# Kernel optimization log

Hardware: AMD Instinct MI355X
Metric: run time of the kernel (lower is better)

Reference implementation:

```python
import jax, jax.numpy as jnp
import numpy as np

BEV_H, BEV_W, ED, HEADS, HD, LEVELS, POINTS, LAYERS = 200, 200, 128, 8, 16, 4, 8, 2
SPATIAL = [(128, 256), (64, 128), (32, 64), (16, 32)]
NV = sum(h * w for h, w in SPATIAL)
NQ = BEV_H * BEV_W
NCLS = 21


def setup_inputs() -> dict:
    key = jax.random.key(0)
    ks = iter(jax.random.split(key, 48))
    r = lambda shape, s=0.02: jax.random.normal(next(ks), shape, jnp.float32) * s
    inp = dict(
        value=r((1, NV, ED), 1.0),
        bev_queries=r((NQ, ED), 0.02),
        bev_pos=r((NQ, ED), 0.02),
        proj_indices=jax.random.randint(next(ks), (1, BEV_H, BEV_W), 0, 250000),
        Wv=r((LAYERS, ED, ED)), bv=jnp.zeros((LAYERS, ED)),
        Woff=r((LAYERS, ED, HEADS * LEVELS * POINTS * 2), 0.01),
        boff=jnp.zeros((LAYERS, HEADS * LEVELS * POINTS * 2)),
        Wattn=r((LAYERS, ED, HEADS * LEVELS * POINTS), 0.01),
        battn=jnp.zeros((LAYERS, HEADS * LEVELS * POINTS)),
        Wout=r((LAYERS, ED, ED)), bout=jnp.zeros((LAYERS, ED)),
        Wf1=r((LAYERS, ED, ED)), bf1=jnp.zeros((LAYERS, ED)),
        Wf2=r((LAYERS, ED, ED)), bf2=jnp.zeros((LAYERS, ED)),
        ln_g=jnp.ones((LAYERS, 2, ED)), ln_b=jnp.zeros((LAYERS, 2, ED)),
        cw1=r((128, ED, 7, 7), 0.01), g1=jnp.ones(128), b1=jnp.zeros(128),
        cw2=r((64, 128, 3, 3), 0.02), g2=jnp.ones(64), b2=jnp.zeros(64),
        cw3=r((48, 64, 3, 3), 0.02), g3=jnp.ones(48), b3=jnp.zeros(48),
        cw4=r((48, 48, 3, 3), 0.02), g4=jnp.ones(48), b4=jnp.zeros(48),
        objw=r((NCLS, 48, 1, 1), 0.05), objb=jnp.zeros(NCLS),
    )
    return inp


def _ln(x, g, b):
    m = x.mean(-1, keepdims=True)
    v = ((x - m) ** 2).mean(-1, keepdims=True)
    return (x - m) * jax.lax.rsqrt(v + 1e-5) * g + b


def _deform_attn(q, value, Wv, bv, Woff, boff, Wattn, battn, Wout, bout, ref):
    # multi-scale deformable attention (Deformable-DETR / BEVFormer core)
    v = (value[0] @ Wv + bv).reshape(NV, HEADS, HD)
    off = (q @ Woff + boff).reshape(NQ, HEADS, LEVELS, POINTS, 2)
    attn = jax.nn.softmax((q @ Wattn + battn).reshape(NQ, HEADS, LEVELS * POINTS), -1)
    attn = attn.reshape(NQ, HEADS, LEVELS, POINTS)
    out = jnp.zeros((HEADS, NQ, HD), jnp.float32)
    start = 0
    for l, (H, W) in enumerate(SPATIAL):
        vl = v[start:start + H * W].transpose(1, 0, 2)  # [HEADS, H*W, HD]
        start += H * W
        # normalized sampling locations in [0,1]
        loc = ref[:, None, None, :] + off[:, :, l] / jnp.array([W, H], jnp.float32)
        x = loc[..., 0] * W - 0.5  # grid_sample align_corners=False convention
        y = loc[..., 1] * H - 0.5  # [NQ, HEADS, POINTS]
        x0 = jnp.floor(x)
        y0 = jnp.floor(y)
        acc = jnp.zeros((HEADS, NQ, POINTS, HD), jnp.float32)
        for dx, dy in ((0, 0), (1, 0), (0, 1), (1, 1)):
            xc = x0 + dx
            yc = y0 + dy
            wgt = (1.0 - jnp.abs(x - xc)) * (1.0 - jnp.abs(y - yc))
            valid = (xc >= 0) & (xc < W) & (yc >= 0) & (yc < H)
            xi = jnp.clip(xc, 0, W - 1).astype(jnp.int32)
            yi = jnp.clip(yc, 0, H - 1).astype(jnp.int32)
            idx = (yi * W + xi).transpose(1, 0, 2)  # [HEADS, NQ, POINTS]
            g = jax.vmap(lambda vh, ih: vh[ih])(vl, idx)  # [HEADS, NQ, POINTS, HD]
            acc = acc + (wgt * valid).transpose(1, 0, 2)[..., None] * g
        out = out + jnp.einsum('nhp,hnpd->hnd', attn[:, :, l], acc)
    return out.transpose(1, 0, 2).reshape(NQ, ED) @ Wout + bout


def _bev_encoder(bev_queries, bev_pos, value, Wv, bv, Woff, boff, Wattn, battn, Wout, bout, Wf1, bf1, Wf2, bf2, ln_g, ln_b):
    gx = (jnp.arange(BEV_W, dtype=jnp.float32) + 0.5) / BEV_W
    gy = (jnp.arange(BEV_H, dtype=jnp.float32) + 0.5) / BEV_H
    ref = jnp.stack(jnp.meshgrid(gx, gy), -1).reshape(NQ, 2)  # (x, y)
    q = bev_queries
    for i in range(LAYERS):  # operation_order: cross_attn, norm, ffn, norm
        a = _deform_attn(q + bev_pos, value, Wv[i], bv[i], Woff[i], boff[i],
                         Wattn[i], battn[i], Wout[i], bout[i], ref)
        q = _ln(q + a, ln_g[i, 0], ln_b[i, 0])
        h = jax.nn.relu(q @ Wf1[i] + bf1[i]) @ Wf2[i] + bf2[i]
        q = _ln(q + h, ln_g[i, 1], ln_b[i, 1])
    return q


def _conv(x, w, p):
    return jax.lax.conv_general_dilated(x, w, (1, 1), [(p, p), (p, p)],
                                        dimension_numbers=('NCHW', 'OIHW', 'NCHW'))


def _bn_relu(x, g, b):
    m = x.mean((0, 2, 3), keepdims=True)
    v = x.var((0, 2, 3), keepdims=True)
    return jax.nn.relu((x - m) * jax.lax.rsqrt(v + 1e-5) * g[None, :, None, None] + b[None, :, None, None])


def reference(value, bev_queries, bev_pos, proj_indices, Wv, bv, Woff, boff, Wattn, battn, Wout, bout, Wf1, bf1, Wf2, bf2, ln_g, ln_b, cw1, g1, b1, cw2, g2, b2, cw3, g3, b3, cw4, g4, b4, objw, objb):
    observed_masks = proj_indices < jnp.max(proj_indices)  # mask_update
    q = _bev_encoder(bev_queries, bev_pos, value, Wv, bv, Woff, boff, Wattn, battn,
                     Wout, bout, Wf1, bf1, Wf2, bf2, ln_g, ln_b)
    mem = q.reshape(1, BEV_H, BEV_W, ED).transpose(0, 3, 1, 2)  # [1, ED, H, W]
    h = _bn_relu(_conv(mem, cw1, 3), g1, b1)
    h = _bn_relu(_conv(h, cw2, 1), g2, b2)
    h = _bn_relu(_conv(h, cw3, 1), g3, b3)
    h = _bn_relu(_conv(h, cw4, 1), g4, b4)
    semmap = _conv(h, objw, 0) + objb[None, :, None, None]
    return semmap, observed_masks
```

## Files before the change

kernel.cpp:

```cpp
#include <hip/hip_runtime.h>
#include <cstdint>
#include <cstddef>

#define NQ 40000
#define EDIM 128
#define NVAL 43520
#define NCLS 21

typedef unsigned short u16;
typedef unsigned int uint;
typedef short bf16x8 __attribute__((ext_vector_type(8)));
typedef float f32x4 __attribute__((ext_vector_type(4)));

__device__ inline u16 f2b(float f) {
    unsigned u = __float_as_uint(f);
    unsigned r = u + 0x7FFF + ((u >> 16) & 1);
    return (u16)(r >> 16);
}
__device__ inline float b2f(u16 v) {
    unsigned u = ((unsigned)v) << 16;
    return __uint_as_float(u);
}
__device__ inline float blo(uint u) { return __uint_as_float(u << 16); }
__device__ inline float bhi(uint u) { return __uint_as_float(u & 0xFFFF0000u); }

__global__ void reduce_max_int(const int* __restrict__ idx, int* __restrict__ mx) {
    int i = blockIdx.x * 256 + threadIdx.x;
    int v = (i < NQ) ? idx[i] : 0;
    for (int o = 32; o > 0; o >>= 1) v = max(v, __shfl_xor(v, o, 64));
    if ((threadIdx.x & 63) == 0) atomicMax(mx, v);
}

__global__ void write_mask(const int* __restrict__ idx, const int* __restrict__ mx,
                           float* __restrict__ out) {
    int i = blockIdx.x * 256 + threadIdx.x;
    if (i >= NQ) return;
    out[i] = (idx[i] < *mx) ? 1.0f : 0.0f;
}

__global__ void cvt_b_k(const float* __restrict__ src, u16* __restrict__ dst, int n8) {
    int i = blockIdx.x * 256 + threadIdx.x;
    if (i >= n8) return;
    const float4 a = ((const float4*)src)[i * 2];
    const float4 b = ((const float4*)src)[i * 2 + 1];
    u16 o[8] = {f2b(a.x), f2b(a.y), f2b(a.z), f2b(a.w), f2b(b.x), f2b(b.y), f2b(b.z), f2b(b.w)};
    ((uint4*)dst)[i] = *(const uint4*)o;
}

__global__ void add2b_k(const float* __restrict__ a, const float* __restrict__ b,
                        u16* __restrict__ c, int n8) {
    int i = blockIdx.x * 256 + threadIdx.x;
    if (i >= n8) return;
    const float4 a0 = ((const float4*)a)[i * 2], a1 = ((const float4*)a)[i * 2 + 1];
    const float4 b0 = ((const float4*)b)[i * 2], b1 = ((const float4*)b)[i * 2 + 1];
    u16 o[8] = {f2b(a0.x + b0.x), f2b(a0.y + b0.y), f2b(a0.z + b0.z), f2b(a0.w + b0.w),
                f2b(a1.x + b1.x), f2b(a1.y + b1.y), f2b(a1.z + b1.z), f2b(a1.w + b1.w)};
    ((uint4*)c)[i] = *(const uint4*)o;
}

__global__ void pack_enc_k(const float* __restrict__ Wv, const float* __restrict__ Woff,
                           const float* __restrict__ Wattn, const float* __restrict__ Wout,
                           const float* __restrict__ Wf1, const float* __restrict__ Wf2,
                           u16* __restrict__ dst) {
    int i = blockIdx.x * 256 + threadIdx.x;
    if (i >= 327680) return;
    int l = i / 163840, r = i % 163840;
    int k = r / 1280, col = r % 1280;
    const float* src; int N; int n; u16* d;
    u16* base = dst + (size_t)l * 163840;
    if (col < 128)       { src = Wv    + (size_t)l * 16384; N = 128; n = col;        d = base;          }
    else if (col < 640)  { src = Woff  + (size_t)l * 65536; N = 512; n = col - 128;  d = base + 16384;  }
    else if (col < 896)  { src = Wattn + (size_t)l * 32768; N = 256; n = col - 640;  d = base + 81920;  }
    else if (col < 1024) { src = Wout  + (size_t)l * 16384; N = 128; n = col - 896;  d = base + 114688; }
    else if (col < 1152) { src = Wf1   + (size_t)l * 16384; N = 128; n = col - 1024; d = base + 131072; }
    else                 { src = Wf2   + (size_t)l * 16384; N = 128; n = col - 1152; d = base + 147456; }
    d[(size_t)n * 128 + k] = f2b(src[(size_t)k * N + n]);
}

__global__ void pack_bias_k(const float* __restrict__ boff, const float* __restrict__ battn,
                            float* __restrict__ dst) {
    int i = blockIdx.x * 256 + threadIdx.x;
    if (i >= 1536) return;
    int l = i / 768, r = i % 768;
    dst[i] = (r < 512) ? boff[(size_t)l * 512 + r] : battn[(size_t)l * 256 + r - 512];
}

__global__ void pack_cw_k(const float* __restrict__ w, u16* __restrict__ wT,
                          int OC, int IC, int KS, int OCp, int ICp) {
    int i = blockIdx.x * 256 + threadIdx.x;
    int tot = KS * KS * OCp * ICp;
    if (i >= tot) return;
    int ic = i % ICp; int r = i / ICp;
    int oc = r % OCp; int tap = r / OCp;
    int ky = tap / KS, kx = tap % KS;
    float v = 0.f;
    if (oc < OC && ic < IC)
        v = w[(((size_t)oc * IC + ic) * KS + ky) * KS + kx];
    wT[i] = f2b(v);
}

__global__ __launch_bounds__(256) void gemm_mfma_k(
        const u16* __restrict__ A, const u16* __restrict__ BT,
        const float* __restrict__ bias, float* __restrict__ Cf,
        u16* __restrict__ Cb, int N, int relu) {
    __shared__ u16 As[64 * 136];
    __shared__ u16 Bs[64 * 136];
    const int m0 = blockIdx.x * 64, n0 = blockIdx.y * 64;
    const int t = threadIdx.x;
#pragma unroll
    for (int ci = t; ci < 1024; ci += 256) {
        int r = ci >> 4, c = ci & 15;
        *(uint4*)&As[r * 136 + c * 8] = *(const uint4*)&A[(size_t)(m0 + r) * 128 + c * 8];
        *(uint4*)&Bs[r * 136 + c * 8] = *(const uint4*)&BT[(size_t)(n0 + r) * 128 + c * 8];
    }
    __syncthreads();
    const int wave = t >> 6, lane = t & 63;
    const int wm = (wave & 1) * 32, wn = (wave >> 1) * 32;
    const int lr = lane & 15, lk = (lane >> 4) * 8;
    f32x4 acc[2][2] = {};
#pragma unroll
    for (int ks = 0; ks < 4; ks++) {
        bf16x8 a0 = *(const bf16x8*)&As[(wm + lr) * 136 + ks * 32 + lk];
        bf16x8 a1 = *(const bf16x8*)&As[(wm + 16 + lr) * 136 + ks * 32 + lk];
        bf16x8 b0 = *(const bf16x8*)&Bs[(wn + lr) * 136 + ks * 32 + lk];
        bf16x8 b1 = *(const bf16x8*)&Bs[(wn + 16 + lr) * 136 + ks * 32 + lk];
        acc[0][0] = __builtin_amdgcn_mfma_f32_16x16x32_bf16(a0, b0, acc[0][0], 0, 0, 0);
        acc[0][1] = __builtin_amdgcn_mfma_f32_16x16x32_bf16(a0, b1, acc[0][1], 0, 0, 0);
        acc[1][0] = __builtin_amdgcn_mfma_f32_16x16x32_bf16(a1, b0, acc[1][0], 0, 0, 0);
        acc[1][1] = __builtin_amdgcn_mfma_f32_16x16x32_bf16(a1, b1, acc[1][1], 0, 0, 0);
    }
    float bj0 = bias[n0 + wn + lr];
    float bj1 = bias[n0 + wn + 16 + lr];
#pragma unroll
    for (int i = 0; i < 2; i++) {
#pragma unroll
        for (int j = 0; j < 2; j++) {
            float bb = j ? bj1 : bj0;
#pragma unroll
            for (int r = 0; r < 4; r++) {
                int ml = wm + i * 16 + (lane >> 4) * 4 + r;
                int nl = wn + j * 16 + lr;
                float v = acc[i][j][r] + bb;
                if (relu) v = fmaxf(v, 0.f);
                size_t o = (size_t)(m0 + ml) * N + n0 + nl;
                if (Cf) Cf[o] = v;
                if (Cb) Cb[o] = f2b(v);
            }
        }
    }
}

template <int KS, int ICP>
__global__ __launch_bounds__(256) void conv4_mfma_k(
        const u16* __restrict__ pimg, const u16* __restrict__ wT,
        float* __restrict__ out, int OCtot) {
    constexpr int PAD = KS / 2;
    constexpr int WIN = 64 + KS - 1;
    constexpr int LDSTR = ICP + 8;
    constexpr int KSTEPS = ICP / 32;
    constexpr int NTAP = KS * KS;
    __shared__ u16 As[WIN * LDSTR];
    const int bx = blockIdx.x;
    const int y = bx >> 2;
    const int xc = bx & 3;
    const int x0 = (xc == 3) ? 136 : xc * 64;
    const int n0 = blockIdx.y * 64;
    const int t = threadIdx.x;
    const int wave = t >> 6, lane = t & 63;
    const int wm = (wave & 1) * 32, wn = (wave >> 1) * 32;
    const int lr = lane & 15, lkq = lane >> 4, lk = lkq * 8;

    f32x4 acc[2][2] = {};
    const u16* wbase = wT + (size_t)n0 * ICP;

    bf16x8 cur0[KSTEPS], cur1[KSTEPS], nxt0[KSTEPS], nxt1[KSTEPS];
#pragma unroll
    for (int ks = 0; ks < KSTEPS; ks++) {
        cur0[ks] = *(const bf16x8*)&wbase[(size_t)(wn + lr) * ICP + ks * 32 + lk];
        cur1[ks] = *(const bf16x8*)&wbase[(size_t)(wn + 16 + lr) * ICP + ks * 32 + lk];
    }

    for (int ky = 0; ky < KS; ky++) {
        __syncthreads();
        const u16* src = pimg + (((size_t)(y + ky + 3 - PAD)) * 208 + (x0 + 3 - PAD)) * ICP;
        for (int ci = t; ci < WIN * (ICP / 8); ci += 256) {
            int r = ci / (ICP / 8), c = ci - r * (ICP / 8);
            *(uint4*)&As[r * LDSTR + c * 8] = *(const uint4*)&src[(size_t)r * ICP + c * 8];
        }
        __syncthreads();
#pragma unroll
        for (int kx = 0; kx < KS; kx++) {
            const int tap = ky * KS + kx;
            if (tap + 1 < NTAP) {
                const u16* wb = wbase + (size_t)(tap + 1) * OCtot * ICP;
#pragma unroll
                for (int ks = 0; ks < KSTEPS; ks++) {
                    nxt0[ks] = *(const bf16x8*)&wb[(size_t)(wn + lr) * ICP + ks * 32 + lk];
                    nxt1[ks] = *(const bf16x8*)&wb[(size_t)(wn + 16 + lr) * ICP + ks * 32 + lk];
                }
            }
#pragma unroll
            for (int ks = 0; ks < KSTEPS; ks++) {
                bf16x8 a0 = *(const bf16x8*)&As[(wm + lr + kx) * LDSTR + ks * 32 + lk];
                bf16x8 a1 = *(const bf16x8*)&As[(wm + 16 + lr + kx) * LDSTR + ks * 32 + lk];
                acc[0][0] = __builtin_amdgcn_mfma_f32_16x16x32_bf16(a0, cur0[ks], acc[0][0], 0, 0, 0);
                acc[0][1] = __builtin_amdgcn_mfma_f32_16x16x32_bf16(a0, cur1[ks], acc[0][1], 0, 0, 0);
                acc[1][0] = __builtin_amdgcn_mfma_f32_16x16x32_bf16(a1, cur0[ks], acc[1][0], 0, 0, 0);
                acc[1][1] = __builtin_amdgcn_mfma_f32_16x16x32_bf16(a1, cur1[ks], acc[1][1], 0, 0, 0);
            }
#pragma unroll
            for (int ks = 0; ks < KSTEPS; ks++) { cur0[ks] = nxt0[ks]; cur1[ks] = nxt1[ks]; }
        }
    }
    const int px0 = y * 200 + x0;
#pragma unroll
    for (int i = 0; i < 2; i++) {
#pragma unroll
        for (int j = 0; j < 2; j++) {
#pragma unroll
            for (int r = 0; r < 4; r++) {
                int ml = wm + i * 16 + lkq * 4 + r;
                int nl = wn + j * 16 + lr;
                out[(size_t)(px0 + ml) * OCtot + n0 + nl] = acc[i][j][r];
            }
        }
    }
}

__global__ __launch_bounds__(256) void deform3_k(
        const u16* __restrict__ v, const u16* __restrict__ oa,
        u16* __restrict__ outb, int q0, int nq) {
    const int t = threadIdx.x;
    const int wq = t >> 6;
    const int lane = t & 63;
    const int s = lane >> 5;
    const int l32 = lane & 31;
    const int h = l32 >> 2;
    const int cl = l32 & 3;
    const int qi = blockIdx.x * 8 + wq * 2 + s;
    if (qi >= nq) return;
    const int gq = q0 + qi;
    const float rx = ((gq % 200) + 0.5f) / 200.f;
    const float ry = ((gq / 200) + 0.5f) / 200.f;

    const uint* lp = (const uint*)(oa + (size_t)qi * 768 + 512 + h * 32);
    float lg[32];
#pragma unroll
    for (int i = 0; i < 16; i++) { uint u = lp[i]; lg[2 * i] = blo(u); lg[2 * i + 1] = bhi(u); }
    float mx = -1e30f;
#pragma unroll
    for (int i = 0; i < 32; i++) mx = fmaxf(mx, lg[i]);
    float ssum = 0.f;
#pragma unroll
    for (int i = 0; i < 32; i++) { lg[i] = __expf(lg[i] - mx); ssum += lg[i]; }
    const float inv = 1.f / ssum;

    const uint* op = (const uint*)(oa + (size_t)qi * 768 + h * 64);

    const int HS[4] = {128, 64, 32, 16};
    const int WS[4] = {256, 128, 64, 32};
    const int ST[4] = {0, 32768, 40960, 43008};
    float a0 = 0.f, a1 = 0.f, a2 = 0.f, a3 = 0.f;
#pragma unroll
    for (int l = 0; l < 4; l++) {
        const int H = HS[l], W = WS[l];
        const float fW = (float)W, fH = (float)H;
        const u16* vb = v + (size_t)ST[l] * 128 + h * 16 + cl * 4;
#pragma unroll
        for (int p = 0; p < 8; p++) {
            uint pr = op[l * 8 + p];
            float ox = blo(pr), oy = bhi(pr);
            float xx = rx * fW + ox - 0.5f;
            float yy = ry * fH + oy - 0.5f;
            float xf = floorf(xx), yf = floorf(yy);
            int ix = (int)xf, iy = (int)yf;
            float fx = xx - xf, fy = yy - yf;
            float aw = lg[l * 8 + p] * inv;
            int x1 = ix + 1, y1 = iy + 1;
            bool vx0 = (unsigned)ix < (unsigned)W;
            bool vx1 = (unsigned)x1 < (unsigned)W;
            bool vy0 = (unsigned)iy < (unsigned)H;
            bool vy1 = (unsigned)y1 < (unsigned)H;
            int cx0 = min(max(ix, 0), W - 1), cx1 = min(max(x1, 0), W - 1);
            int cy0 = min(max(iy, 0), H - 1), cy1 = min(max(y1, 0), H - 1);
            float w00 = (vx0 && vy0) ? (1.f - fx) * (1.f - fy) * aw : 0.f;
            float w10 = (vx1 && vy0) ? fx * (1.f - fy) * aw : 0.f;
            float w01 = (vx0 && vy1) ? (1.f - fx) * fy * aw : 0.f;
            float w11 = (vx1 && vy1) ? fx * fy * aw : 0.f;
            uint2 u00 = *(const uint2*)(vb + (size_t)(cy0 * W + cx0) * 128);
            uint2 u10 = *(const uint2*)(vb + (size_t)(cy0 * W + cx1) * 128);
            uint2 u01 = *(const uint2*)(vb + (size_t)(cy1 * W + cx0) * 128);
            uint2 u11 = *(const uint2*)(vb + (size_t)(cy1 * W + cx1) * 128);
            a0 = fmaf(w00, blo(u00.x), a0); a1 = fmaf(w00, bhi(u00.x), a1);
            a2 = fmaf(w00, blo(u00.y), a2); a3 = fmaf(w00, bhi(u00.y), a3);
            a0 = fmaf(w10, blo(u10.x), a0); a1 = fmaf(w10, bhi(u10.x), a1);
            a2 = fmaf(w10, blo(u10.y), a2); a3 = fmaf(w10, bhi(u10.y), a3);
            a0 = fmaf(w01, blo(u01.x), a0); a1 = fmaf(w01, bhi(u01.x), a1);
            a2 = fmaf(w01, blo(u01.y), a2); a3 = fmaf(w01, bhi(u01.y), a3);
            a0 = fmaf(w11, blo(u11.x), a0); a1 = fmaf(w11, bhi(u11.x), a1);
            a2 = fmaf(w11, blo(u11.y), a2); a3 = fmaf(w11, bhi(u11.y), a3);
        }
    }
    uint2 o;
    o.x = (uint)f2b(a0) | ((uint)f2b(a1) << 16);
    o.y = (uint)f2b(a2) | ((uint)f2b(a3) << 16);
    *(uint2*)(outb + (size_t)gq * 128 + h * 16 + cl * 4) = o;
}

__global__ __launch_bounds__(256) void add_ln_k(
        float* __restrict__ q, const float* __restrict__ a,
        const float* __restrict__ g, const float* __restrict__ b,
        u16* __restrict__ qb) {
    const int row = blockIdx.x * 4 + (threadIdx.x >> 6);
    const int lane = threadIdx.x & 63;
    float s0 = q[(size_t)row * 128 + lane] + a[(size_t)row * 128 + lane];
    float s1 = q[(size_t)row * 128 + 64 + lane] + a[(size_t)row * 128 + 64 + lane];
    float sum = s0 + s1;
    for (int o = 32; o > 0; o >>= 1) sum += __shfl_xor(sum, o, 64);
    float mean = sum * (1.f / 128.f);
    float d0 = s0 - mean, d1 = s1 - mean;
    float vs = d0 * d0 + d1 * d1;
    for (int o = 32; o > 0; o >>= 1) vs += __shfl_xor(vs, o, 64);
    float inv = rsqrtf(vs * (1.f / 128.f) + 1e-5f);
    float o0 = d0 * inv * g[lane] + b[lane];
    float o1 = d1 * inv * g[64 + lane] + b[64 + lane];
    q[(size_t)row * 128 + lane] = o0;
    q[(size_t)row * 128 + 64 + lane] = o1;
    qb[(size_t)row * 128 + lane] = f2b(o0);
    qb[(size_t)row * 128 + 64 + lane] = f2b(o1);
}

__global__ void fill_pimg2_k(const u16* __restrict__ qb, u16* __restrict__ pimg) {
    int i = blockIdx.x * 256 + threadIdx.x;
    if (i >= 685568) return;
    int pp = i >> 4, c8 = i & 15;
    int py = pp / 208, px = pp - py * 208;
    uint4 val = {0u, 0u, 0u, 0u};
    if (py >= 3 && py < 203 && px >= 3 && px < 203)
        val = ((const uint4*)qb)[((size_t)((py - 3) * 200 + (px - 3))) * 16 + c8];
    ((uint4*)pimg)[i] = val;
}

__global__ __launch_bounds__(256) void bn_stats2_k(const float* __restrict__ x,
                                                   float* __restrict__ acc,
                                                   int cSh, int ppb) {
    const int t = threadIdx.x;
    const int Cp = 1 << cSh;
    const int c = t & (Cp - 1);
    const int sub = t >> cSh;
    const int nsub = 256 >> cSh;
    float s = 0.f, s2 = 0.f;
    const int pbase = blockIdx.x * ppb;
    for (int i = sub; i < ppb; i += nsub) {
        float v = x[(size_t)(pbase + i) * Cp + c];
        s += v; s2 += v * v;
    }
    __shared__ float ls[256], ls2[256];
    ls[t] = s; ls2[t] = s2;
    __syncthreads();
    if (t < Cp) {
        for (int k = 1; k < nsub; k++) { s += ls[t + k * Cp]; s2 += ls2[t + k * Cp]; }
        atomicAdd(&acc[2 * t], s);
        atomicAdd(&acc[2 * t + 1], s2);
    }
}

__global__ void bn_fin_k(const float* __restrict__ acc, float* __restrict__ mv, int C) {
    int t = threadIdx.x;
    if (t >= C) return;
    float m = acc[2 * t] * (1.f / 40000.f);
    float var = acc[2 * t + 1] * (1.f / 40000.f) - m * m;
    mv[2 * t] = m;
    mv[2 * t + 1] = rsqrtf(var + 1e-5f);
}

__global__ void bn_apply_pad2_k(const float* __restrict__ x, const float* __restrict__ mv,
                                const float* __restrict__ g, const float* __restrict__ b,
                                u16* __restrict__ outp, int cSh, int Creal) {
    int i = blockIdx.x * 256 + threadIdx.x;
    int Cp = 1 << cSh;
    if (i >= 206 * 208 * Cp) return;
    int c = i & (Cp - 1);
    int pp = i >> cSh;
    int py = pp / 208, px = pp - py * 208;
    float v = 0.f;
    if (c < Creal && py >= 3 && py < 203 && px >= 3 && px < 203) {
        int p = (py - 3) * 200 + (px - 3);
        v = fmaxf((x[(size_t)p * Cp + c] - mv[2 * c]) * mv[2 * c + 1] * g[c] + b[c], 0.f);
    }
    outp[i] = f2b(v);
}

__global__ void bn_apply2_k(const float* __restrict__ x, const float* __restrict__ mv,
                            const float* __restrict__ g, const float* __restrict__ b,
                            u16* __restrict__ outb, int cSh, int Creal) {
    int i = blockIdx.x * 256 + threadIdx.x;
    int Cp = 1 << cSh;
    if (i >= 40000 * Cp) return;
    int c = i & (Cp - 1);
    float v = 0.f;
    if (c < Creal) v = fmaxf((x[i] - mv[2 * c]) * mv[2 * c + 1] * g[c] + b[c], 0.f);
    outb[i] = f2b(v);
}

__global__ void obj_conv_k(const u16* __restrict__ in, const float* __restrict__ w,
                           const float* __restrict__ bias, float* __restrict__ out) {
    int p = blockIdx.x * 256 + threadIdx.x;
    if (p >= 40000) return;
    float xin[48];
#pragma unroll
    for (int c = 0; c < 48; c++) xin[c] = b2f(in[(size_t)p * 64 + c]);
    for (int o = 0; o < NCLS; o++) {
        float acc = bias[o];
#pragma unroll
        for (int c = 0; c < 48; c++) acc += xin[c] * w[o * 48 + c];
        out[(size_t)o * 40000 + p] = acc;
    }
}

extern "C" void kernel_launch(void* const* d_in, const int* in_sizes, int n_in,
                              void* d_out, int out_size, void* d_ws, size_t ws_size,
                              hipStream_t stream) {
    const float* value   = (const float*)d_in[0];
    const float* bev_q   = (const float*)d_in[1];
    const float* bev_pos = (const float*)d_in[2];
    const int*   proj    = (const int*)d_in[3];
    const float* Wv      = (const float*)d_in[4];
    const float* bv      = (const float*)d_in[5];
    const float* Woff    = (const float*)d_in[6];
    const float* boff    = (const float*)d_in[7];
    const float* Wattn   = (const float*)d_in[8];
    const float* battn   = (const float*)d_in[9];
    const float* Wout    = (const float*)d_in[10];
    const float* bout    = (const float*)d_in[11];
    const float* Wf1     = (const float*)d_in[12];
    const float* bf1     = (const float*)d_in[13];
    const float* Wf2     = (const float*)d_in[14];
    const float* bf2     = (const float*)d_in[15];
    const float* ln_g    = (const float*)d_in[16];
    const float* ln_b    = (const float*)d_in[17];
    const float* cw1     = (const float*)d_in[18];
    const float* g1      = (const float*)d_in[19];
    const float* b1      = (const float*)d_in[20];
    const float* cw2     = (const float*)d_in[21];
    const float* g2      = (const float*)d_in[22];
    const float* b2      = (const float*)d_in[23];
    const float* cw3     = (const float*)d_in[24];
    const float* g3      = (const float*)d_in[25];
    const float* b3      = (const float*)d_in[26];
    const float* cw4     = (const float*)d_in[27];
    const float* g4      = (const float*)d_in[28];
    const float* b4      = (const float*)d_in[29];
    const float* objw    = (const float*)d_in[30];
    const float* objb    = (const float*)d_in[31];
    float* out = (float*)d_out;

    float* WSb = (float*)d_ws;
    float* q     = WSb + 0;
    u16*   qb    = (u16*)(WSb + 5120000);
    u16*   qpb   = (u16*)(WSb + 7680000);
    u16*   valb  = (u16*)(WSb + 10240000);
    u16*   vbufb = (u16*)(WSb + 13025280);
    u16*   fb    = (u16*)(WSb + 15810560);
    float* tmp   = WSb + 18882560;
    u16*   aob   = (u16*)(WSb + 24002560);
    u16*   hb    = (u16*)(WSb + 26562560);
    u16*   wenc  = (u16*)(WSb + 29122560);
    u16*   wcv   = (u16*)(WSb + 29286400);
    float* bnacc = WSb + 29761536;
    float* bnmv  = WSb + 29762048;
    int*   maxi  = (int*)(WSb + 29762304);
    float* fbias = WSb + 29762308;

    u16*   pimg = (u16*)(WSb + 10240000);
    float* c1f  = tmp;
    u16*   c1b  = (u16*)(WSb + 13025280);
    float* c2f  = WSb + 0;
    u16*   c2b  = (u16*)(WSb + 5120000);
    float* c3f  = WSb + 2560000;
    u16*   c3b  = (u16*)(WSb + 7680000);
    float* c4f  = WSb + 0;
    u16*   c4b  = (u16*)(WSb + 15810560);

    const size_t L = 163840;
    u16* WvT[2]; u16* WoffT[2]; u16* WoutT[2]; u16* Wf1T[2]; u16* Wf2T[2];
    for (int l = 0; l < 2; l++) {
        u16* base = wenc + l * L;
        WvT[l]    = base;
        WoffT[l]  = base + 16384;
        WoutT[l]  = base + 114688;
        Wf1T[l]   = base + 131072;
        Wf2T[l]   = base + 147456;
    }
    u16* w1T = wcv;
    u16* w2T = wcv + 802816;
    u16* w3T = wcv + 876544;
    u16* w4T = wcv + 913408;

    hipMemsetAsync(maxi, 0, sizeof(int), stream);
    reduce_max_int<<<157, 256, 0, stream>>>(proj, maxi);
    write_mask<<<157, 256, 0, stream>>>(proj, maxi, out + 840000);

    pack_enc_k<<<1280, 256, 0, stream>>>(Wv, Woff, Wattn, Wout, Wf1, Wf2, wenc);
    pack_bias_k<<<6, 256, 0, stream>>>(boff, battn, fbias);
    pack_cw_k<<<3136, 256, 0, stream>>>(cw1, w1T, 128, 128, 7, 128, 128);
    pack_cw_k<<<288, 256, 0, stream>>>(cw2, w2T, 64, 128, 3, 64, 128);
    pack_cw_k<<<144, 256, 0, stream>>>(cw3, w3T, 48, 64, 3, 64, 64);
    pack_cw_k<<<144, 256, 0, stream>>>(cw4, w4T, 48, 48, 3, 64, 64);
    cvt_b_k<<<2720, 256, 0, stream>>>(value, valb, NVAL * 128 / 8);

    hipMemcpyAsync(q, bev_q, (size_t)NQ * EDIM * sizeof(float),
                   hipMemcpyDeviceToDevice, stream);
    const int CH0 = 19968, CH1 = 20032;
    for (int l = 0; l < 2; l++) {
        gemm_mfma_k<<<dim3(680, 2), 256, 0, stream>>>(
            valb, WvT[l], bv + (size_t)l * 128, nullptr, vbufb, 128, 0);
        add2b_k<<<2500, 256, 0, stream>>>(q, bev_pos, qpb, NQ * 128 / 8);
        for (int cidx = 0; cidx < 2; cidx++) {
            int qs = cidx ? CH0 : 0;
            int nq = cidx ? CH1 : CH0;
            gemm_mfma_k<<<dim3(nq / 64, 12), 256, 0, stream>>>(
                qpb + (size_t)qs * 128, WoffT[l], fbias + (size_t)l * 768,
                nullptr, fb, 768, 0);
            deform3_k<<<nq / 8, 256, 0, stream>>>(vbufb, fb, aob, qs, nq);
        }
        gemm_mfma_k<<<dim3(625, 2), 256, 0, stream>>>(
            aob, WoutT[l], bout + (size_t)l * 128, tmp, nullptr, 128, 0);
        add_ln_k<<<10000, 256, 0, stream>>>(q, tmp, ln_g + (size_t)(l * 2 + 0) * 128,
                                            ln_b + (size_t)(l * 2 + 0) * 128, qb);
        gemm_mfma_k<<<dim3(625, 2), 256, 0, stream>>>(
            qb, Wf1T[l], bf1 + (size_t)l * 128, nullptr, hb, 128, 1);
        gemm_mfma_k<<<dim3(625, 2), 256, 0, stream>>>(
            hb, Wf2T[l], bf2 + (size_t)l * 128, tmp, nullptr, 128, 0);
        add_ln_k<<<10000, 256, 0, stream>>>(q, tmp, ln_g + (size_t)(l * 2 + 1) * 128,
                                            ln_b + (size_t)(l * 2 + 1) * 128, qb);
    }

    fill_pimg2_k<<<2678, 256, 0, stream>>>(qb, pimg);

    conv4_mfma_k<7, 128><<<dim3(800, 2), 256, 0, stream>>>(pimg, w1T, c1f, 128);
    hipMemsetAsync(bnacc, 0, 512 * sizeof(float), stream);
    bn_stats2_k<<<125, 256, 0, stream>>>(c1f, bnacc, 7, 320);
    bn_fin_k<<<1, 128, 0, stream>>>(bnacc, bnmv, 128);
    bn_apply_pad2_k<<<21424, 256, 0, stream>>>(c1f, bnmv, g1, b1, c1b, 7, 128);

    conv4_mfma_k<3, 128><<<dim3(800, 1), 256, 0, stream>>>(c1b, w2T, c2f, 64);
    hipMemsetAsync(bnacc, 0, 512 * sizeof(float), stream);
    bn_stats2_k<<<125, 256, 0, stream>>>(c2f, bnacc, 6, 320);
    bn_fin_k<<<1, 64, 0, stream>>>(bnacc, bnmv, 64);
    bn_apply_pad2_k<<<10712, 256, 0, stream>>>(c2f, bnmv, g2, b2, c2b, 6, 64);

    conv4_mfma_k<3, 64><<<dim3(800, 1), 256, 0, stream>>>(c2b, w3T, c3f, 64);
    hipMemsetAsync(bnacc, 0, 512 * sizeof(float), stream);
    bn_stats2_k<<<125, 256, 0, stream>>>(c3f, bnacc, 6, 320);
    bn_fin_k<<<1, 48, 0, stream>>>(bnacc, bnmv, 48);
    bn_apply_pad2_k<<<10712, 256, 0, stream>>>(c3f, bnmv, g3, b3, c3b, 6, 48);

    conv4_mfma_k<3, 64><<<dim3(800, 1), 256, 0, stream>>>(c3b, w4T, c4f, 64);
    hipMemsetAsync(bnacc, 0, 512 * sizeof(float), stream);
    bn_stats2_k<<<125, 256, 0, stream>>>(c4f, bnacc, 6, 320);
    bn_fin_k<<<1, 48, 0, stream>>>(bnacc, bnmv, 48);
    bn_apply2_k<<<10000, 256, 0, stream>>>(c4f, bnmv, g4, b4, c4b, 6, 48);

    obj_conv_k<<<157, 256, 0, stream>>>(c4b, objw, objb, out);
}
```

Before: 1.161 ms.

## Process two output rows per conv block and stage weights in double-buffered LDS

The implicit-GEMM conv kernel now computes two output rows per block (grid halved). Each wave owns one row and 64 pixels by 32 output channels. Per-tap weight tiles are now loaded cooperatively into a double-buffered LDS buffer instead of each wave loading its own fragments into registers, so each weight tile is fetched once per block and reused across both rows. The cost is more LDS use, an extra barrier per tap, fewer blocks for occupancy and more accumulator registers per thread.

```diff
diff --git a/kernel.cpp b/kernel.cpp
--- a/kernel.cpp
+++ b/kernel.cpp
@@ -151,75 +151,98 @@
 }
 
 template <int KS, int ICP>
-__global__ __launch_bounds__(256) void conv4_mfma_k(
+__global__ __launch_bounds__(256) void conv5_mfma_k(
         const u16* __restrict__ pimg, const u16* __restrict__ wT,
         float* __restrict__ out, int OCtot) {
     constexpr int PAD = KS / 2;
     constexpr int WIN = 64 + KS - 1;
-    constexpr int LDSTR = ICP + 8;
+    constexpr int STR = ICP + 8;
     constexpr int KSTEPS = ICP / 32;
     constexpr int NTAP = KS * KS;
-    __shared__ u16 As[WIN * LDSTR];
+    constexpr int ACH = WIN * (ICP / 8);
+    constexpr int NB = ICP / 32;
+    __shared__ u16 As[2 * WIN * STR];
+    __shared__ u16 Bs[2 * 64 * STR];
     const int bx = blockIdx.x;
-    const int y = bx >> 2;
+    const int yp = (bx >> 2) * 2;
     const int xc = bx & 3;
     const int x0 = (xc == 3) ? 136 : xc * 64;
     const int n0 = blockIdx.y * 64;
     const int t = threadIdx.x;
     const int wave = t >> 6, lane = t & 63;
-    const int wm = (wave & 1) * 32, wn = (wave >> 1) * 32;
+    const int row = wave >> 1;
+    const int wn = (wave & 1) * 32;
     const int lr = lane & 15, lkq = lane >> 4, lk = lkq * 8;
 
-    f32x4 acc[2][2] = {};
+    f32x4 acc[4][2] = {};
     const u16* wbase = wT + (size_t)n0 * ICP;
 
-    bf16x8 cur0[KSTEPS], cur1[KSTEPS], nxt0[KSTEPS], nxt1[KSTEPS];
-#pragma unroll
-    for (int ks = 0; ks < KSTEPS; ks++) {
-        cur0[ks] = *(const bf16x8*)&wbase[(size_t)(wn + lr) * ICP + ks * 32 + lk];
-        cur1[ks] = *(const bf16x8*)&wbase[(size_t)(wn + 16 + lr) * ICP + ks * 32 + lk];
-    }
+    uint4 breg[NB];
+    int bro[NB], bco[NB];
+#pragma unroll
+    for (int k = 0; k < NB; k++) {
+        int ci = t + k * 256;
+        bro[k] = ci / (ICP / 8);
+        bco[k] = ci - bro[k] * (ICP / 8);
+    }
+#pragma unroll
+    for (int k = 0; k < NB; k++)
+        breg[k] = *(const uint4*)&wbase[(size_t)bro[k] * ICP + bco[k] * 8];
+#pragma unroll
+    for (int k = 0; k < NB; k++)
+        *(uint4*)&Bs[(size_t)bro[k] * STR + bco[k] * 8] = breg[k];
 
     for (int ky = 0; ky < KS; ky++) {
         __syncthreads();
-        const u16* src = pimg + (((size_t)(y + ky + 3 - PAD)) * 208 + (x0 + 3 - PAD)) * ICP;
-        for (int ci = t; ci < WIN * (ICP / 8); ci += 256) {
-            int r = ci / (ICP / 8), c = ci - r * (ICP / 8);
-            *(uint4*)&As[r * LDSTR + c * 8] = *(const uint4*)&src[(size_t)r * ICP + c * 8];
+        {
+            const u16* s0 = pimg + (((size_t)(yp + ky + 3 - PAD)) * 208 + (x0 + 3 - PAD)) * ICP;
+            const u16* s1 = pimg + (((size_t)(yp + 1 + ky + 3 - PAD)) * 208 + (x0 + 3 - PAD)) * ICP;
+            for (int ci = t; ci < 2 * ACH; ci += 256) {
+                int w2 = ci / ACH, rem = ci - w2 * ACH;
+                int r = rem / (ICP / 8), c = rem - r * (ICP / 8);
+                const u16* s = w2 ? s1 : s0;
+                *(uint4*)&As[(size_t)(w2 * WIN + r) * STR + c * 8] =
+                    *(const uint4*)&s[(size_t)r * ICP + c * 8];
+            }
         }
-        __syncthreads();
-#pragma unroll
         for (int kx = 0; kx < KS; kx++) {
             const int tap = ky * KS + kx;
+            __syncthreads();
             if (tap + 1 < NTAP) {
-                const u16* wb = wbase + (size_t)(tap + 1) * OCtot * ICP;
-#pragma unroll
-                for (int ks = 0; ks < KSTEPS; ks++) {
-                    nxt0[ks] = *(const bf16x8*)&wb[(size_t)(wn + lr) * ICP + ks * 32 + lk];
-                    nxt1[ks] = *(const bf16x8*)&wb[(size_t)(wn + 16 + lr) * ICP + ks * 32 + lk];
+                const u16* ws = wbase + (size_t)(tap + 1) * OCtot * ICP;
+#pragma unroll
+                for (int k = 0; k < NB; k++)
+                    breg[k] = *(const uint4*)&ws[(size_t)bro[k] * ICP + bco[k] * 8];
+            }
+            const u16* ab = &As[((size_t)row * WIN + kx) * STR];
+            const u16* bb = &Bs[(size_t)((tap & 1) * 64 + wn) * STR];
+#pragma unroll
+            for (int ks = 0; ks < KSTEPS; ks++) {
+                bf16x8 b0 = *(const bf16x8*)&bb[(size_t)lr * STR + ks * 32 + lk];
+                bf16x8 b1 = *(const bf16x8*)&bb[(size_t)(lr + 16) * STR + ks * 32 + lk];
+#pragma unroll
+                for (int i = 0; i < 4; i++) {
+                    bf16x8 a = *(const bf16x8*)&ab[(size_t)(lr + i * 16) * STR + ks * 32 + lk];
+                    acc[i][0] = __builtin_amdgcn_mfma_f32_16x16x32_bf16(a, b0, acc[i][0], 0, 0, 0);
+                    acc[i][1] = __builtin_amdgcn_mfma_f32_16x16x32_bf16(a, b1, acc[i][1], 0, 0, 0);
                 }
             }
-#pragma unroll
-            for (int ks = 0; ks < KSTEPS; ks++) {
-                bf16x8 a0 = *(const bf16x8*)&As[(wm + lr + kx) * LDSTR + ks * 32 + lk];
-                bf16x8 a1 = *(const bf16x8*)&As[(wm + 16 + lr + kx) * LDSTR + ks * 32 + lk];
-                acc[0][0] = __builtin_amdgcn_mfma_f32_16x16x32_bf16(a0, cur0[ks], acc[0][0], 0, 0, 0);
-                acc[0][1] = __builtin_amdgcn_mfma_f32_16x16x32_bf16(a0, cur1[ks], acc[0][1], 0, 0, 0);
-                acc[1][0] = __builtin_amdgcn_mfma_f32_16x16x32_bf16(a1, cur0[ks], acc[1][0], 0, 0, 0);
-                acc[1][1] = __builtin_amdgcn_mfma_f32_16x16x32_bf16(a1, cur1[ks], acc[1][1], 0, 0, 0);
+            if (tap + 1 < NTAP) {
+                u16* bd = &Bs[(size_t)(((tap + 1) & 1) * 64) * STR];
+#pragma unroll
+                for (int k = 0; k < NB; k++)
+                    *(uint4*)&bd[(size_t)bro[k] * STR + bco[k] * 8] = breg[k];
             }
-#pragma unroll
-            for (int ks = 0; ks < KSTEPS; ks++) { cur0[ks] = nxt0[ks]; cur1[ks] = nxt1[ks]; }
         }
     }
-    const int px0 = y * 200 + x0;
-#pragma unroll
-    for (int i = 0; i < 2; i++) {
+    const int px0 = (yp + row) * 200 + x0;
+#pragma unroll
+    for (int i = 0; i < 4; i++) {
 #pragma unroll
         for (int j = 0; j < 2; j++) {
 #pragma unroll
             for (int r = 0; r < 4; r++) {
-                int ml = wm + i * 16 + lkq * 4 + r;
+                int ml = i * 16 + lkq * 4 + r;
                 int nl = wn + j * 16 + lr;
                 out[(size_t)(px0 + ml) * OCtot + n0 + nl] = acc[i][j][r];
             }
@@ -538,25 +561,25 @@
 
     fill_pimg2_k<<<2678, 256, 0, stream>>>(qb, pimg);
 
-    conv4_mfma_k<7, 128><<<dim3(800, 2), 256, 0, stream>>>(pimg, w1T, c1f, 128);
+    conv5_mfma_k<7, 128><<<dim3(400, 2), 256, 0, stream>>>(pimg, w1T, c1f, 128);
     hipMemsetAsync(bnacc, 0, 512 * sizeof(float), stream);
     bn_stats2_k<<<125, 256, 0, stream>>>(c1f, bnacc, 7, 320);
     bn_fin_k<<<1, 128, 0, stream>>>(bnacc, bnmv, 128);
     bn_apply_pad2_k<<<21424, 256, 0, stream>>>(c1f, bnmv, g1, b1, c1b, 7, 128);
 
-    conv4_mfma_k<3, 128><<<dim3(800, 1), 256, 0, stream>>>(c1b, w2T, c2f, 64);
+    conv5_mfma_k<3, 128><<<dim3(400, 1), 256, 0, stream>>>(c1b, w2T, c2f, 64);
     hipMemsetAsync(bnacc, 0, 512 * sizeof(float), stream);
     bn_stats2_k<<<125, 256, 0, stream>>>(c2f, bnacc, 6, 320);
     bn_fin_k<<<1, 64, 0, stream>>>(bnacc, bnmv, 64);
     bn_apply_pad2_k<<<10712, 256, 0, stream>>>(c2f, bnmv, g2, b2, c2b, 6, 64);
 
-    conv4_mfma_k<3, 64><<<dim3(800, 1), 256, 0, stream>>>(c2b, w3T, c3f, 64);
+    conv5_mfma_k<3, 64><<<dim3(400, 1), 256, 0, stream>>>(c2b, w3T, c3f, 64);
     hipMemsetAsync(bnacc, 0, 512 * sizeof(float), stream);
     bn_stats2_k<<<125, 256, 0, stream>>>(c3f, bnacc, 6, 320);
     bn_fin_k<<<1, 48, 0, stream>>>(bnacc, bnmv, 48);
     bn_apply_pad2_k<<<10712, 256, 0, stream>>>(c3f, bnmv, g3, b3, c3b, 6, 48);
 
-    conv4_mfma_k<3, 64><<<dim3(800, 1), 256, 0, stream>>>(c3b, w4T, c4f, 64);
+    conv5_mfma_k<3, 64><<<dim3(400, 1), 256, 0, stream>>>(c3b, w4T, c4f, 64);
     hipMemsetAsync(bnacc, 0, 512 * sizeof(float), stream);
     bn_stats2_k<<<125, 256, 0, stream>>>(c4f, bnacc, 6, 320);
     bn_fin_k<<<1, 48, 0, stream>>>(bnacc, bnmv, 48);
```

Result: faster. 1.024 ms (-11.8%).
